# Kernel optimization log

Measured on AMD Instinct MI355X. Metric: run time of the kernel, lower is better.

## Reference

```python
import jax, jax.numpy as jnp
import numpy as np

HIDDEN = 2048
INTER = 8192
RANK = 16
SPARSITY_RATIO = 0.5
MAINTAIN_CHANNELS = 10


def setup_inputs() -> dict:
    key = jax.random.key(0)
    ks = jax.random.split(key, 7)
    B, S = 4, 2048
    x1 = jax.random.normal(ks[0], (B, S, HIDDEN), dtype=jnp.float32)
    # Linear weights stored transposed (in_features, out_features), bias=False
    w_up = jax.random.normal(ks[1], (HIDDEN, INTER), dtype=jnp.float32) / np.sqrt(HIDDEN)
    w_up_lora_a = jax.random.normal(ks[2], (HIDDEN, RANK), dtype=jnp.float32) / np.sqrt(HIDDEN)
    w_up_lora_b = jax.random.normal(ks[3], (RANK, INTER), dtype=jnp.float32) / np.sqrt(RANK)
    w_down = jax.random.normal(ks[4], (INTER, HIDDEN), dtype=jnp.float32) / np.sqrt(INTER)
    w_down_lora_a = jax.random.normal(ks[5], (INTER, RANK), dtype=jnp.float32) / np.sqrt(INTER)
    w_down_lora_b = jax.random.normal(ks[6], (RANK, HIDDEN), dtype=jnp.float32) / np.sqrt(RANK)
    return {
        "x1": x1,
        "w_up": w_up,
        "w_up_lora_a": w_up_lora_a,
        "w_up_lora_b": w_up_lora_b,
        "w_down": w_down,
        "w_down_lora_a": w_down_lora_a,
        "w_down_lora_b": w_down_lora_b,
    }


def reference(x1, w_up, w_up_lora_a, w_up_lora_b, w_down, w_down_lora_a, w_down_lora_b):
    # up projection: dense + low-rank LoRA
    y1 = x1 @ w_up + (x1 @ w_up_lora_a) @ w_up_lora_b          # [B, S, I]
    x2 = jax.nn.relu(y1)                                        # activation_forward='relu'
    # down projection: dense + low-rank LoRA
    y2 = x2 @ w_down + (x2 @ w_down_lora_a) @ w_down_lora_b    # [B, S, H]
    # sparse-save path: per-channel zero counts, keep k channels with FEWEST zeros
    zero_counts = jnp.sum(x2 == 0, axis=-2)                     # [B, I]
    k = min(int(SPARSITY_RATIO * x2.shape[-1]), MAINTAIN_CHANNELS)
    _, topk_indices = jax.lax.top_k(-zero_counts, k)            # smallest counts -> [B, k]
    # per-batch gather of selected channels (replaces Python loop in original)
    x2_save = jnp.take_along_axis(x2, topk_indices[:, None, :], axis=-1)  # [B, S, k]
    return y2, x2_save
```

## Files before the change

### kernel.cpp

```cpp
#include <hip/hip_runtime.h>
#include <stdint.h>

#define HIDDEN 2048
#define INTER 8192
#define RANK 16
#define BATCH 4
#define SEQ 2048
#define MROWS (BATCH * SEQ)
#define KSAVE 10
#define FIXCAP (1u << 18)
#define FIX_TAU 1.2e-4f
#define NHALF 4096

typedef unsigned short u16;
typedef __attribute__((ext_vector_type(8))) __bf16 bf16x8;
typedef __attribute__((ext_vector_type(4))) float f32x4;

__device__ __forceinline__ float bf16_to_f32(u16 h) {
    return __uint_as_float(((unsigned int)h) << 16);
}
__device__ __forceinline__ u16 f32_to_bf16(float f) {
    unsigned int u = __float_as_uint(f);
    u += 0x7fffu + ((u >> 16) & 1u);
    return (u16)(u >> 16);
}
__device__ __forceinline__ void split_bf16(float v, u16& h, u16& l) {
    h = f32_to_bf16(v);
    l = f32_to_bf16(v - bf16_to_f32(h));
}

#define TILE_SH (128 * 32)

__device__ __forceinline__ int swz_chunk(int r, int c) {
    return r * 4 + (c ^ ((r >> 1) & 3));
}

__device__ __forceinline__ void stage_tile(const u16* g, int ldk, u16* lds, int wid, int lane) {
#pragma unroll
    for (int h = 0; h < 2; ++h) {
        int ch = h * 256 + wid * 64 + lane;
        int r = ch >> 2;
        int c = (ch & 3) ^ ((r >> 1) & 3);
        const u16* src = g + (size_t)r * ldk + c * 8;
        u16* dst = lds + (size_t)(h * 256 + wid * 64) * 8;
        __builtin_amdgcn_global_load_lds(
            (const __attribute__((address_space(1))) void*)src,
            (__attribute__((address_space(3))) void*)dst, 16, 0, 0);
    }
}

__device__ __forceinline__ bf16x8 read_frag(const u16* lds, int r, int q) {
    return *(const bf16x8*)(lds + swz_chunk(r, q) * 8);
}

__global__ __launch_bounds__(256) void gemm_up_mfma2(
    const float* __restrict__ x1,
    const u16* __restrict__ wth, const u16* __restrict__ wtl,
    const float* __restrict__ t1, const float* __restrict__ upB,
    u16* __restrict__ x2, unsigned* __restrict__ fixctr, unsigned* __restrict__ fixlist,
    int noff)
{
    __shared__ u16 Ah[TILE_SH], Al[TILE_SH], Bh[TILE_SH], Bl[TILE_SH];
    int tid = threadIdx.x, lane = tid & 63, wid = tid >> 6;
    int wr = wid >> 1, wc = wid & 1;
    int col = lane & 15, q = lane >> 4;

    int bid = blockIdx.y * gridDim.x + blockIdx.x;
    int g = bid >> 9, within = bid & 511;
    int nb = g * 8 + (within & 7);
    int mb = within >> 3;
    int m0 = mb * 128, n0l = nb * 128, n0g = noff + n0l;

    f32x4 acc[4][4];
#pragma unroll
    for (int i = 0; i < 4; ++i)
#pragma unroll
        for (int j = 0; j < 4; ++j) acc[i][j] = (f32x4){0.f, 0.f, 0.f, 0.f};

    const float* ga = x1 + (size_t)m0 * HIDDEN;
    const u16* gb_h = wth + (size_t)n0l * HIDDEN;
    const u16* gb_l = wtl + (size_t)n0l * HIDDEN;
    int f4 = tid & 7;
    int rA = tid >> 3;

    for (int k0 = 0; k0 < HIDDEN; k0 += 32) {
        stage_tile(gb_h + k0, HIDDEN, Bh, wid, lane);
        stage_tile(gb_l + k0, HIDDEN, Bl, wid, lane);
        float4 v[4];
#pragma unroll
        for (int h = 0; h < 4; ++h)
            v[h] = *(const float4*)(ga + (size_t)(rA + h * 32) * HIDDEN + k0 + f4 * 4);
#pragma unroll
        for (int h = 0; h < 4; ++h) {
            int r = rA + h * 32;
            unsigned hx0 = __float_as_uint(v[h].x) & 0xffff0000u;
            unsigned hx1 = __float_as_uint(v[h].y) & 0xffff0000u;
            unsigned hx2 = __float_as_uint(v[h].z) & 0xffff0000u;
            unsigned hx3 = __float_as_uint(v[h].w) & 0xffff0000u;
            float l0 = v[h].x - __uint_as_float(hx0);
            float l1 = v[h].y - __uint_as_float(hx1);
            float l2 = v[h].z - __uint_as_float(hx2);
            float l3 = v[h].w - __uint_as_float(hx3);
            unsigned lo0 = __float_as_uint(l0) & 0xffff0000u;
            unsigned lo1 = __float_as_uint(l1) & 0xffff0000u;
            unsigned lo2 = __float_as_uint(l2) & 0xffff0000u;
            unsigned lo3 = __float_as_uint(l3) & 0xffff0000u;
            uint2 hp = {(hx0 >> 16) | hx1, (hx2 >> 16) | hx3};
            uint2 lp = {(lo0 >> 16) | lo1, (lo2 >> 16) | lo3};
            int pos = swz_chunk(r, f4 >> 1) * 8 + (f4 & 1) * 4;
            *(uint2*)(Ah + pos) = hp;
            *(uint2*)(Al + pos) = lp;
        }
        __syncthreads();
        bf16x8 ah[4], al[4];
#pragma unroll
        for (int i = 0; i < 4; ++i) {
            int r = wr * 64 + i * 16 + col;
            ah[i] = read_frag(Ah, r, q);
            al[i] = read_frag(Al, r, q);
        }
#pragma unroll
        for (int j = 0; j < 4; ++j) {
            int r = wc * 64 + j * 16 + col;
            bf16x8 bh = read_frag(Bh, r, q);
            bf16x8 bl = read_frag(Bl, r, q);
#pragma unroll
            for (int i = 0; i < 4; ++i) {
                acc[i][j] = __builtin_amdgcn_mfma_f32_16x16x32_bf16(ah[i], bh, acc[i][j], 0, 0, 0);
                acc[i][j] = __builtin_amdgcn_mfma_f32_16x16x32_bf16(al[i], bh, acc[i][j], 0, 0, 0);
                acc[i][j] = __builtin_amdgcn_mfma_f32_16x16x32_bf16(ah[i], bl, acc[i][j], 0, 0, 0);
            }
        }
        __syncthreads();
    }

    for (int idx = tid; idx < 128 * 32; idx += 256) {
        int r = idx >> 5, c16 = idx & 31;
        float tv = (c16 < RANK) ? t1[(size_t)(m0 + r) * RANK + c16] : 0.f;
        float uv = (c16 < RANK) ? upB[(size_t)c16 * INTER + n0g + r] : 0.f;
        u16 th, tl2, uh, ul;
        split_bf16(tv, th, tl2);
        split_bf16(uv, uh, ul);
        int pos = swz_chunk(r, c16 >> 3) * 8 + (c16 & 7);
        Ah[pos] = th; Al[pos] = tl2; Bh[pos] = uh; Bl[pos] = ul;
    }
    __syncthreads();
    {
        bf16x8 ah[4], al[4];
#pragma unroll
        for (int i = 0; i < 4; ++i) {
            int r = wr * 64 + i * 16 + col;
            ah[i] = read_frag(Ah, r, q);
            al[i] = read_frag(Al, r, q);
        }
#pragma unroll
        for (int j = 0; j < 4; ++j) {
            int r = wc * 64 + j * 16 + col;
            bf16x8 bh = read_frag(Bh, r, q);
            bf16x8 bl = read_frag(Bl, r, q);
#pragma unroll
            for (int i = 0; i < 4; ++i) {
                acc[i][j] = __builtin_amdgcn_mfma_f32_16x16x32_bf16(ah[i], bh, acc[i][j], 0, 0, 0);
                acc[i][j] = __builtin_amdgcn_mfma_f32_16x16x32_bf16(al[i], bh, acc[i][j], 0, 0, 0);
                acc[i][j] = __builtin_amdgcn_mfma_f32_16x16x32_bf16(ah[i], bl, acc[i][j], 0, 0, 0);
            }
        }
    }

#pragma unroll
    for (int i = 0; i < 4; ++i)
#pragma unroll
        for (int j = 0; j < 4; ++j) {
            int n = n0g + wc * 64 + j * 16 + col;
#pragma unroll
            for (int reg = 0; reg < 4; ++reg) {
                int m = m0 + wr * 64 + i * 16 + q * 4 + reg;
                float v = acc[i][j][reg];
                if (fabsf(v) < FIX_TAU) {
                    unsigned slot = atomicAdd(fixctr, 1u);
                    if (slot < FIXCAP) fixlist[slot] = ((unsigned)m << 13) | (unsigned)n;
                }
                float rv = v > 0.f ? v : 0.f;
                x2[(size_t)m * INTER + n] = f32_to_bf16(rv);
            }
        }
}

__global__ __launch_bounds__(256) void gemm_down_mfma(
    const u16* __restrict__ x2, const u16* __restrict__ wdt,
    const float* __restrict__ t2, const float* __restrict__ dnB,
    float* __restrict__ out)
{
    __shared__ u16 As[TILE_SH], Bs[TILE_SH];
    int tid = threadIdx.x, lane = tid & 63, wid = tid >> 6;
    int wr = wid >> 1, wc = wid & 1;
    int col = lane & 15, q = lane >> 4;
    int m0 = blockIdx.y * 128, n0 = blockIdx.x * 128;

    f32x4 acc[4][4];
#pragma unroll
    for (int i = 0; i < 4; ++i)
#pragma unroll
        for (int j = 0; j < 4; ++j) acc[i][j] = (f32x4){0.f, 0.f, 0.f, 0.f};

    const u16* ga = x2 + (size_t)m0 * INTER;
    const u16* gb = wdt + (size_t)n0 * INTER;

    for (int k0 = 0; k0 < INTER; k0 += 32) {
        stage_tile(ga + k0, INTER, As, wid, lane);
        stage_tile(gb + k0, INTER, Bs, wid, lane);
        __syncthreads();
        bf16x8 af[4];
#pragma unroll
        for (int i = 0; i < 4; ++i) af[i] = read_frag(As, wr * 64 + i * 16 + col, q);
#pragma unroll
        for (int j = 0; j < 4; ++j) {
            bf16x8 bf = read_frag(Bs, wc * 64 + j * 16 + col, q);
#pragma unroll
            for (int i = 0; i < 4; ++i)
                acc[i][j] = __builtin_amdgcn_mfma_f32_16x16x32_bf16(af[i], bf, acc[i][j], 0, 0, 0);
        }
        __syncthreads();
    }

    for (int idx = tid; idx < 128 * 32; idx += 256) {
        int r = idx >> 5, c16 = idx & 31;
        float tv = (c16 < RANK) ? t2[(size_t)(m0 + r) * RANK + c16] : 0.f;
        float uv = (c16 < RANK) ? dnB[(size_t)c16 * HIDDEN + n0 + r] : 0.f;
        int pos = swz_chunk(r, c16 >> 3) * 8 + (c16 & 7);
        As[pos] = f32_to_bf16(tv);
        Bs[pos] = f32_to_bf16(uv);
    }
    __syncthreads();
    {
        bf16x8 af[4];
#pragma unroll
        for (int i = 0; i < 4; ++i) af[i] = read_frag(As, wr * 64 + i * 16 + col, q);
#pragma unroll
        for (int j = 0; j < 4; ++j) {
            bf16x8 bf = read_frag(Bs, wc * 64 + j * 16 + col, q);
#pragma unroll
            for (int i = 0; i < 4; ++i)
                acc[i][j] = __builtin_amdgcn_mfma_f32_16x16x32_bf16(af[i], bf, acc[i][j], 0, 0, 0);
        }
    }
#pragma unroll
    for (int i = 0; i < 4; ++i)
#pragma unroll
        for (int j = 0; j < 4; ++j) {
            int n = n0 + wc * 64 + j * 16 + col;
#pragma unroll
            for (int reg = 0; reg < 4; ++reg) {
                int m = m0 + wr * 64 + i * 16 + q * 4 + reg;
                out[(size_t)m * HIDDEN + n] = acc[i][j][reg];
            }
        }
}

__global__ __launch_bounds__(256) void fixup_kernel(
    const float* __restrict__ x1, const float* __restrict__ w_up,
    const float* __restrict__ t1, const float* __restrict__ upB,
    const unsigned* __restrict__ fixctr, const unsigned* __restrict__ fixlist,
    u16* __restrict__ x2)
{
    unsigned n_items = *fixctr;
    if (n_items > FIXCAP) n_items = FIXCAP;
    int lane = threadIdx.x & 63;
    int gwave = blockIdx.x * 4 + (threadIdx.x >> 6);
    int nwaves = gridDim.x * 4;
    for (unsigned it = gwave; it < n_items; it += nwaves) {
        unsigned code = fixlist[it];
        int m = code >> 13, n = code & 8191;
        float s = 0.f;
        const float* xr = x1 + (size_t)m * HIDDEN;
        for (int k = lane; k < HIDDEN; k += 64)
            s = fmaf(xr[k], w_up[(size_t)k * INTER + n], s);
#pragma unroll
        for (int off = 32; off > 0; off >>= 1) s += __shfl_down(s, off);
        if (lane == 0) {
            float lo = 0.f;
#pragma unroll
            for (int r = 0; r < RANK; ++r)
                lo = fmaf(t1[(size_t)m * RANK + r], upB[(size_t)r * INTER + n], lo);
            float y = s + lo;
            x2[(size_t)m * INTER + n] = f32_to_bf16(y > 0.f ? y : 0.f);
        }
    }
}

template <bool SPLIT>
__global__ __launch_bounds__(256) void transpose_cvt(
    const float* __restrict__ in, u16* __restrict__ outh, u16* __restrict__ outl,
    int R, int C)
{
    __shared__ float t[32][33];
    int x = threadIdx.x & 31, y = threadIdx.x >> 5;
    int r0 = blockIdx.y * 32, c0 = blockIdx.x * 32;
#pragma unroll
    for (int p = 0; p < 4; ++p)
        t[y + p * 8][x] = in[(size_t)(r0 + y + p * 8) * C + c0 + x];
    __syncthreads();
#pragma unroll
    for (int p = 0; p < 4; ++p) {
        float v = t[x][y + p * 8];
        u16 h = f32_to_bf16(v);
        outh[(size_t)(c0 + y + p * 8) * R + r0 + x] = h;
        if (SPLIT)
            outl[(size_t)(c0 + y + p * 8) * R + r0 + x] = f32_to_bf16(v - bf16_to_f32(h));
    }
}

__global__ __launch_bounds__(256) void rowdot16_f32(
    const float* __restrict__ X, const float* __restrict__ A,
    float* __restrict__ T, int K)
{
    __shared__ float red[256][RANK + 1];
    int m = blockIdx.x;
    const float* xr = X + (size_t)m * K;
    float acc[RANK];
#pragma unroll
    for (int r = 0; r < RANK; ++r) acc[r] = 0.f;
    for (int k = threadIdx.x; k < K; k += 256) {
        float xv = xr[k];
        const float* ar = A + (size_t)k * RANK;
#pragma unroll
        for (int r = 0; r < RANK; ++r) acc[r] = fmaf(xv, ar[r], acc[r]);
    }
#pragma unroll
    for (int r = 0; r < RANK; ++r) red[threadIdx.x][r] = acc[r];
    __syncthreads();
    for (int off = 128; off > 0; off >>= 1) {
        if (threadIdx.x < off) {
#pragma unroll
            for (int r = 0; r < RANK; ++r)
                red[threadIdx.x][r] += red[threadIdx.x + off][r];
        }
        __syncthreads();
    }
    if (threadIdx.x < RANK) T[(size_t)m * RANK + threadIdx.x] = red[0][threadIdx.x];
}

__global__ __launch_bounds__(256) void rowdot16_bf16(
    const u16* __restrict__ X, const float* __restrict__ A,
    float* __restrict__ T, int K)
{
    __shared__ float red[256][RANK + 1];
    int m = blockIdx.x;
    const u16* xr = X + (size_t)m * K;
    float acc[RANK];
#pragma unroll
    for (int r = 0; r < RANK; ++r) acc[r] = 0.f;
    for (int k = threadIdx.x; k < K; k += 256) {
        float xv = bf16_to_f32(xr[k]);
        const float* ar = A + (size_t)k * RANK;
#pragma unroll
        for (int r = 0; r < RANK; ++r) acc[r] = fmaf(xv, ar[r], acc[r]);
    }
#pragma unroll
    for (int r = 0; r < RANK; ++r) red[threadIdx.x][r] = acc[r];
    __syncthreads();
    for (int off = 128; off > 0; off >>= 1) {
        if (threadIdx.x < off) {
#pragma unroll
            for (int r = 0; r < RANK; ++r)
                red[threadIdx.x][r] += red[threadIdx.x + off][r];
        }
        __syncthreads();
    }
    if (threadIdx.x < RANK) T[(size_t)m * RANK + threadIdx.x] = red[0][threadIdx.x];
}

#define BM 128
#define BN 128
#define BK 16
#define TM 8

__global__ __launch_bounds__(256) void gemm_up_f32(
    const float* __restrict__ A, const float* __restrict__ B,
    const float* __restrict__ Tl, const float* __restrict__ Bl,
    u16* __restrict__ C, int M, int N, int K)
{
    __shared__ float As[BK][BM + 4];
    __shared__ float Bs[BK][BN];
    int tid = threadIdx.x;
    int tx = tid % 16, ty = tid / 16;
    int m0 = blockIdx.y * BM, n0 = blockIdx.x * BN;
    const float* Ab = A + (size_t)m0 * K;
    const float* Bb = B + n0;
    float acc[TM][8];
#pragma unroll
    for (int i = 0; i < TM; ++i)
#pragma unroll
        for (int j = 0; j < 8; ++j) acc[i][j] = 0.f;

    int arow = tid >> 2, acol = (tid & 3) * 4;
    int brow = tid >> 5, bcol = (tid & 31) * 4;

    for (int k0 = 0; k0 < K; k0 += BK) {
#pragma unroll
        for (int h = 0; h < 2; ++h) {
            int r = arow + h * 64;
            float4 v = *(const float4*)(Ab + (size_t)r * K + k0 + acol);
            As[acol + 0][r] = v.x; As[acol + 1][r] = v.y;
            As[acol + 2][r] = v.z; As[acol + 3][r] = v.w;
        }
#pragma unroll
        for (int h = 0; h < 2; ++h) {
            int r = brow + h * 8;
            float4 v = *(const float4*)(Bb + (size_t)(k0 + r) * N + bcol);
            *(float4*)&Bs[r][bcol] = v;
        }
        __syncthreads();
#pragma unroll
        for (int kk = 0; kk < BK; ++kk) {
            float a[TM], b[8];
#pragma unroll
            for (int i = 0; i < TM; i += 4) *(float4*)&a[i] = *(const float4*)&As[kk][ty * TM + i];
            *(float4*)&b[0] = *(const float4*)&Bs[kk][tx * 4];
            *(float4*)&b[4] = *(const float4*)&Bs[kk][64 + tx * 4];
#pragma unroll
            for (int i = 0; i < TM; ++i)
#pragma unroll
                for (int j = 0; j < 8; ++j)
                    acc[i][j] = fmaf(a[i], b[j], acc[i][j]);
        }
        __syncthreads();
    }
#pragma unroll
    for (int r = 0; r < RANK; ++r) {
        float bv[8];
#pragma unroll
        for (int j = 0; j < 4; ++j) {
            bv[j]     = Bl[(size_t)r * N + n0 + tx * 4 + j];
            bv[4 + j] = Bl[(size_t)r * N + n0 + 64 + tx * 4 + j];
        }
#pragma unroll
        for (int i = 0; i < TM; ++i) {
            float tv = Tl[(size_t)(m0 + ty * TM + i) * RANK + r];
#pragma unroll
            for (int j = 0; j < 8; ++j) acc[i][j] = fmaf(tv, bv[j], acc[i][j]);
        }
    }
#pragma unroll
    for (int i = 0; i < TM; ++i) {
        int m = m0 + ty * TM + i;
        float v[8];
#pragma unroll
        for (int j = 0; j < 8; ++j) { float x = acc[i][j]; v[j] = x > 0.f ? x : 0.f; }
        uint2 p0, p1;
        p0.x = (unsigned)f32_to_bf16(v[0]) | ((unsigned)f32_to_bf16(v[1]) << 16);
        p0.y = (unsigned)f32_to_bf16(v[2]) | ((unsigned)f32_to_bf16(v[3]) << 16);
        p1.x = (unsigned)f32_to_bf16(v[4]) | ((unsigned)f32_to_bf16(v[5]) << 16);
        p1.y = (unsigned)f32_to_bf16(v[6]) | ((unsigned)f32_to_bf16(v[7]) << 16);
        *(uint2*)(C + (size_t)m * N + n0 + tx * 4) = p0;
        *(uint2*)(C + (size_t)m * N + n0 + 64 + tx * 4) = p1;
    }
}

__global__ __launch_bounds__(256) void gemm_down_f32(
    const u16* __restrict__ A, const float* __restrict__ B,
    const float* __restrict__ Tl, const float* __restrict__ Bl,
    float* __restrict__ C, int M, int N, int K)
{
    __shared__ float As[BK][BM + 4];
    __shared__ float Bs[BK][BN];
    int tid = threadIdx.x;
    int tx = tid % 16, ty = tid / 16;
    int m0 = blockIdx.y * BM, n0 = blockIdx.x * BN;
    const u16* Ab = A + (size_t)m0 * K;
    const float* Bb = B + n0;
    float acc[TM][8];
#pragma unroll
    for (int i = 0; i < TM; ++i)
#pragma unroll
        for (int j = 0; j < 8; ++j) acc[i][j] = 0.f;

    int arow = tid >> 1, ahalf = (tid & 1) * 8;
    int brow = tid >> 5, bcol = (tid & 31) * 4;

    for (int k0 = 0; k0 < K; k0 += BK) {
        {
            uint4 v = *(const uint4*)(Ab + (size_t)arow * K + k0 + ahalf);
            unsigned int w_[4] = {v.x, v.y, v.z, v.w};
#pragma unroll
            for (int qq = 0; qq < 4; ++qq) {
                As[ahalf + 2 * qq + 0][arow] = bf16_to_f32((u16)(w_[qq] & 0xffffu));
                As[ahalf + 2 * qq + 1][arow] = bf16_to_f32((u16)(w_[qq] >> 16));
            }
        }
#pragma unroll
        for (int h = 0; h < 2; ++h) {
            int r = brow + h * 8;
            float4 v = *(const float4*)(Bb + (size_t)(k0 + r) * N + bcol);
            *(float4*)&Bs[r][bcol] = v;
        }
        __syncthreads();
#pragma unroll
        for (int kk = 0; kk < BK; ++kk) {
            float a[TM], b[8];
#pragma unroll
            for (int i = 0; i < TM; i += 4) *(float4*)&a[i] = *(const float4*)&As[kk][ty * TM + i];
            *(float4*)&b[0] = *(const float4*)&Bs[kk][tx * 4];
            *(float4*)&b[4] = *(const float4*)&Bs[kk][64 + tx * 4];
#pragma unroll
            for (int i = 0; i < TM; ++i)
#pragma unroll
                for (int j = 0; j < 8; ++j)
                    acc[i][j] = fmaf(a[i], b[j], acc[i][j]);
        }
        __syncthreads();
    }
#pragma unroll
    for (int r = 0; r < RANK; ++r) {
        float bv[8];
#pragma unroll
        for (int j = 0; j < 4; ++j) {
            bv[j]     = Bl[(size_t)r * N + n0 + tx * 4 + j];
            bv[4 + j] = Bl[(size_t)r * N + n0 + 64 + tx * 4 + j];
        }
#pragma unroll
        for (int i = 0; i < TM; ++i) {
            float tv = Tl[(size_t)(m0 + ty * TM + i) * RANK + r];
#pragma unroll
            for (int j = 0; j < 8; ++j) acc[i][j] = fmaf(tv, bv[j], acc[i][j]);
        }
    }
#pragma unroll
    for (int i = 0; i < TM; ++i) {
        int m = m0 + ty * TM + i;
        *(float4*)(C + (size_t)m * N + n0 + tx * 4)      = *(float4*)&acc[i][0];
        *(float4*)(C + (size_t)m * N + n0 + 64 + tx * 4) = *(float4*)&acc[i][4];
    }
}

__global__ __launch_bounds__(256) void count_zeros(
    const u16* __restrict__ X2, int* __restrict__ counts)
{
    int i = blockIdx.x * 256 + threadIdx.x;
    int b = blockIdx.y;
    int s0 = blockIdx.z * 256;
    const u16* p = X2 + ((size_t)(b * SEQ + s0)) * INTER + i;
    int c = 0;
    for (int s = 0; s < 256; ++s) c += (p[(size_t)s * INTER] == 0) ? 1 : 0;
    atomicAdd(&counts[b * INTER + i], c);
}

__global__ __launch_bounds__(256) void topk10(
    const int* __restrict__ counts, int* __restrict__ topidx)
{
    __shared__ int keys[INTER];
    __shared__ int red[256];
    int b = blockIdx.x;
    for (int i = threadIdx.x; i < INTER; i += 256)
        keys[i] = (counts[b * INTER + i] << 13) | i;
    __syncthreads();
    for (int sel = 0; sel < KSAVE; ++sel) {
        int best = 0x7fffffff;
        for (int i = threadIdx.x; i < INTER; i += 256)
            best = min(best, keys[i]);
        red[threadIdx.x] = best;
        __syncthreads();
        for (int off = 128; off > 0; off >>= 1) {
            if (threadIdx.x < off) red[threadIdx.x] = min(red[threadIdx.x], red[threadIdx.x + off]);
            __syncthreads();
        }
        int bestkey = red[0];
        if (threadIdx.x == 0) {
            topidx[b * KSAVE + sel] = bestkey & 0x1fff;
            keys[bestkey & 0x1fff] = 0x7fffffff;
        }
        __syncthreads();
    }
}

__global__ __launch_bounds__(256) void gather_save(
    const u16* __restrict__ X2, const int* __restrict__ topidx,
    float* __restrict__ out2)
{
    int t = blockIdx.x * 256 + threadIdx.x;
    if (t >= BATCH * SEQ * KSAVE) return;
    int j = t % KSAVE;
    int s = (t / KSAVE) % SEQ;
    int b = t / (KSAVE * SEQ);
    int idx = topidx[b * KSAVE + j];
    out2[t] = bf16_to_f32(X2[((size_t)(b * SEQ + s)) * INTER + idx]);
}

extern "C" void kernel_launch(void* const* d_in, const int* in_sizes, int n_in,
                              void* d_out, int out_size, void* d_ws, size_t ws_size,
                              hipStream_t stream)
{
    const float* x1   = (const float*)d_in[0];
    const float* w_up = (const float*)d_in[1];
    const float* upA  = (const float*)d_in[2];
    const float* upB  = (const float*)d_in[3];
    const float* w_dn = (const float*)d_in[4];
    const float* dnA  = (const float*)d_in[5];
    const float* dnB  = (const float*)d_in[6];
    float* out = (float*)d_out;
    char* ws = (char*)d_ws;

    const size_t X2B   = (size_t)MROWS * INTER * 2;
    const size_t WHALF = (size_t)NHALF * HIDDEN * 2;
    const size_t WSPL  = (size_t)HIDDEN * INTER * 2;
    const size_t TB    = (size_t)MROWS * RANK * 4;
    const size_t CNTB  = (size_t)BATCH * INTER * 4;

    size_t fast_need = X2B + 2 * WHALF + 2 * TB + CNTB + 512 + 4 * (size_t)FIXCAP;
    size_t mid_need  = X2B + WSPL + 2 * TB + CNTB + 512;

    u16* x2 = (u16*)ws;
    size_t off = X2B;

    if (ws_size >= fast_need) {
        u16* wth = (u16*)(ws + off);            off += WHALF;
        u16* wtl = (u16*)(ws + off);            off += WHALF;
        float* t1 = (float*)(ws + off);         off += TB;
        float* t2 = (float*)(ws + off);         off += TB;
        int* counts = (int*)(ws + off);         off += CNTB;
        int* topidx = (int*)(ws + off);         off += 256;
        unsigned* fixctr = (unsigned*)(ws + off); off += 256;
        unsigned* fixlist = (unsigned*)(ws + off);
        u16* wdt = wth;

        hipMemsetAsync(counts, 0, CNTB, stream);
        hipMemsetAsync(fixctr, 0, 4, stream);

        rowdot16_f32<<<MROWS, 256, 0, stream>>>(x1, upA, t1, HIDDEN);

        for (int half = 0; half < 2; ++half) {
            int noff = half * NHALF;
            transpose_cvt<true><<<dim3(NHALF / 32, HIDDEN / 32), 256, 0, stream>>>(
                w_up + noff, wth, wtl, HIDDEN, INTER);
            gemm_up_mfma2<<<dim3(NHALF / 128, MROWS / 128), 256, 0, stream>>>(
                x1, wth, wtl, t1, upB, x2, fixctr, fixlist, noff);
        }
        fixup_kernel<<<256, 256, 0, stream>>>(x1, w_up, t1, upB, fixctr, fixlist, x2);

        count_zeros<<<dim3(INTER / 256, BATCH, SEQ / 256), 256, 0, stream>>>(x2, counts);
        topk10<<<BATCH, 256, 0, stream>>>(counts, topidx);
        gather_save<<<(BATCH * SEQ * KSAVE + 255) / 256, 256, 0, stream>>>(
            x2, topidx, out + (size_t)MROWS * HIDDEN);

        transpose_cvt<false><<<dim3(HIDDEN / 32, INTER / 32), 256, 0, stream>>>(
            w_dn, wdt, nullptr, INTER, HIDDEN);
        rowdot16_bf16<<<MROWS, 256, 0, stream>>>(x2, dnA, t2, INTER);
        gemm_down_mfma<<<dim3(HIDDEN / 128, MROWS / 128), 256, 0, stream>>>(
            x2, wdt, t2, dnB, out);
    } else if (ws_size >= mid_need) {
        u16* wdt = (u16*)(ws + off);            off += WSPL;
        float* t1 = (float*)(ws + off);         off += TB;
        float* t2 = (float*)(ws + off);         off += TB;
        int* counts = (int*)(ws + off);         off += CNTB;
        int* topidx = (int*)(ws + off);

        hipMemsetAsync(counts, 0, CNTB, stream);
        rowdot16_f32<<<MROWS, 256, 0, stream>>>(x1, upA, t1, HIDDEN);
        gemm_up_f32<<<dim3(INTER / BN, MROWS / BM), 256, 0, stream>>>(
            x1, w_up, t1, upB, x2, MROWS, INTER, HIDDEN);
        count_zeros<<<dim3(INTER / 256, BATCH, SEQ / 256), 256, 0, stream>>>(x2, counts);
        topk10<<<BATCH, 256, 0, stream>>>(counts, topidx);
        gather_save<<<(BATCH * SEQ * KSAVE + 255) / 256, 256, 0, stream>>>(
            x2, topidx, out + (size_t)MROWS * HIDDEN);
        transpose_cvt<false><<<dim3(HIDDEN / 32, INTER / 32), 256, 0, stream>>>(
            w_dn, wdt, nullptr, INTER, HIDDEN);
        rowdot16_bf16<<<MROWS, 256, 0, stream>>>(x2, dnA, t2, INTER);
        gemm_down_mfma<<<dim3(HIDDEN / 128, MROWS / 128), 256, 0, stream>>>(
            x2, wdt, t2, dnB, out);
    } else {
        float* t1 = (float*)(ws + off);         off += TB;
        float* t2 = (float*)(ws + off);         off += TB;
        int* counts = (int*)(ws + off);         off += CNTB;
        int* topidx = (int*)(ws + off);

        hipMemsetAsync(counts, 0, CNTB, stream);
        rowdot16_f32<<<MROWS, 256, 0, stream>>>(x1, upA, t1, HIDDEN);
        gemm_up_f32<<<dim3(INTER / BN, MROWS / BM), 256, 0, stream>>>(
            x1, w_up, t1, upB, x2, MROWS, INTER, HIDDEN);
        count_zeros<<<dim3(INTER / 256, BATCH, SEQ / 256), 256, 0, stream>>>(x2, counts);
        topk10<<<BATCH, 256, 0, stream>>>(counts, topidx);
        gather_save<<<(BATCH * SEQ * KSAVE + 255) / 256, 256, 0, stream>>>(
            x2, topidx, out + (size_t)MROWS * HIDDEN);
        rowdot16_bf16<<<MROWS, 256, 0, stream>>>(x2, dnA, t2, INTER);
        gemm_down_f32<<<dim3(HIDDEN / BN, MROWS / BM), 256, 0, stream>>>(
            x2, w_dn, t2, dnB, out, MROWS, HIDDEN, INTER);
    }
}
```

Measured before the change: 1.996 ms.

## Widen MFMA GEMM tiles to 128x256 with 8 waves and fuse zero counting

Both the up and down MFMA GEMMs move from 128x128 tiles with 4 waves to 128x256 tiles with 8 waves (512 threads). Each staged A tile is now reused across twice as many output columns, which cuts global and LDS traffic for the activation operand. Zero counting is folded into the up-GEMM epilogue with shuffle reductions and atomics, and the fixup kernel adjusts counts when it flips a sign, so the separate count_zeros pass over x2 is removed. The bf16 rowdot kernel is vectorized to load 8 elements per thread. The costs are more LDS per block, fewer blocks in the grid, and extra atomics in the epilogue.

Result: slower. 2.258 ms (+13.1%).

```diff
diff --git a/kernel.cpp b/kernel.cpp
--- a/kernel.cpp
+++ b/kernel.cpp
@@ -35,14 +35,16 @@
     return r * 4 + (c ^ ((r >> 1) & 3));
 }
 
-__device__ __forceinline__ void stage_tile(const u16* g, int ldk, u16* lds, int wid, int lane) {
-#pragma unroll
-    for (int h = 0; h < 2; ++h) {
-        int ch = h * 256 + wid * 64 + lane;
+template <int NCH>
+__device__ __forceinline__ void stage_tileN(const u16* g, int ldk, u16* lds, int tid) {
+    int wid = tid >> 6, lane = tid & 63;
+#pragma unroll
+    for (int c0 = 0; c0 < NCH; c0 += 512) {
+        int ch = c0 + wid * 64 + lane;
         int r = ch >> 2;
         int c = (ch & 3) ^ ((r >> 1) & 3);
         const u16* src = g + (size_t)r * ldk + c * 8;
-        u16* dst = lds + (size_t)(h * 256 + wid * 64) * 8;
+        u16* dst = lds + (size_t)(c0 + wid * 64) * 8;
         __builtin_amdgcn_global_load_lds(
             (const __attribute__((address_space(1))) void*)src,
             (__attribute__((address_space(3))) void*)dst, 16, 0, 0);
@@ -53,23 +55,25 @@
     return *(const bf16x8*)(lds + swz_chunk(r, q) * 8);
 }
 
-__global__ __launch_bounds__(256) void gemm_up_mfma2(
+__global__ __launch_bounds__(512) void gemm_up_mfma3(
     const float* __restrict__ x1,
     const u16* __restrict__ wth, const u16* __restrict__ wtl,
     const float* __restrict__ t1, const float* __restrict__ upB,
-    u16* __restrict__ x2, unsigned* __restrict__ fixctr, unsigned* __restrict__ fixlist,
+    u16* __restrict__ x2, int* __restrict__ counts,
+    unsigned* __restrict__ fixctr, unsigned* __restrict__ fixlist,
     int noff)
 {
-    __shared__ u16 Ah[TILE_SH], Al[TILE_SH], Bh[TILE_SH], Bl[TILE_SH];
+    __shared__ u16 Ah[TILE_SH], Al[TILE_SH];
+    __shared__ u16 Bh[2 * TILE_SH], Bl[2 * TILE_SH];
     int tid = threadIdx.x, lane = tid & 63, wid = tid >> 6;
-    int wr = wid >> 1, wc = wid & 1;
+    int wr = wid >> 2, wc = wid & 3;
     int col = lane & 15, q = lane >> 4;
 
     int bid = blockIdx.y * gridDim.x + blockIdx.x;
-    int g = bid >> 9, within = bid & 511;
-    int nb = g * 8 + (within & 7);
-    int mb = within >> 3;
-    int m0 = mb * 128, n0l = nb * 128, n0g = noff + n0l;
+    int g = bid >> 8, within = bid & 255;
+    int nb = g * 4 + (within & 3);
+    int mb = within >> 2;
+    int m0 = mb * 128, n0l = nb * 256, n0g = noff + n0l;
 
     f32x4 acc[4][4];
 #pragma unroll
@@ -84,30 +88,27 @@
     int rA = tid >> 3;
 
     for (int k0 = 0; k0 < HIDDEN; k0 += 32) {
-        stage_tile(gb_h + k0, HIDDEN, Bh, wid, lane);
-        stage_tile(gb_l + k0, HIDDEN, Bl, wid, lane);
-        float4 v[4];
-#pragma unroll
-        for (int h = 0; h < 4; ++h)
-            v[h] = *(const float4*)(ga + (size_t)(rA + h * 32) * HIDDEN + k0 + f4 * 4);
-#pragma unroll
-        for (int h = 0; h < 4; ++h) {
-            int r = rA + h * 32;
-            unsigned hx0 = __float_as_uint(v[h].x) & 0xffff0000u;
-            unsigned hx1 = __float_as_uint(v[h].y) & 0xffff0000u;
-            unsigned hx2 = __float_as_uint(v[h].z) & 0xffff0000u;
-            unsigned hx3 = __float_as_uint(v[h].w) & 0xffff0000u;
-            float l0 = v[h].x - __uint_as_float(hx0);
-            float l1 = v[h].y - __uint_as_float(hx1);
-            float l2 = v[h].z - __uint_as_float(hx2);
-            float l3 = v[h].w - __uint_as_float(hx3);
+        stage_tileN<1024>(gb_h + k0, HIDDEN, Bh, tid);
+        stage_tileN<1024>(gb_l + k0, HIDDEN, Bl, tid);
+#pragma unroll
+        for (int h = 0; h < 2; ++h) {
+            int row = rA + h * 64;
+            float4 v = *(const float4*)(ga + (size_t)row * HIDDEN + k0 + f4 * 4);
+            unsigned hx0 = __float_as_uint(v.x) & 0xffff0000u;
+            unsigned hx1 = __float_as_uint(v.y) & 0xffff0000u;
+            unsigned hx2 = __float_as_uint(v.z) & 0xffff0000u;
+            unsigned hx3 = __float_as_uint(v.w) & 0xffff0000u;
+            float l0 = v.x - __uint_as_float(hx0);
+            float l1 = v.y - __uint_as_float(hx1);
+            float l2 = v.z - __uint_as_float(hx2);
+            float l3 = v.w - __uint_as_float(hx3);
             unsigned lo0 = __float_as_uint(l0) & 0xffff0000u;
             unsigned lo1 = __float_as_uint(l1) & 0xffff0000u;
             unsigned lo2 = __float_as_uint(l2) & 0xffff0000u;
             unsigned lo3 = __float_as_uint(l3) & 0xffff0000u;
             uint2 hp = {(hx0 >> 16) | hx1, (hx2 >> 16) | hx3};
             uint2 lp = {(lo0 >> 16) | lo1, (lo2 >> 16) | lo3};
-            int pos = swz_chunk(r, f4 >> 1) * 8 + (f4 & 1) * 4;
+            int pos = swz_chunk(row, f4 >> 1) * 8 + (f4 & 1) * 4;
             *(uint2*)(Ah + pos) = hp;
             *(uint2*)(Al + pos) = lp;
         }
@@ -121,9 +122,9 @@
         }
 #pragma unroll
         for (int j = 0; j < 4; ++j) {
-            int r = wc * 64 + j * 16 + col;
-            bf16x8 bh = read_frag(Bh, r, q);
-            bf16x8 bl = read_frag(Bl, r, q);
+            int rr = wc * 64 + j * 16 + col;
+            bf16x8 bh = read_frag(Bh, rr, q);
+            bf16x8 bl = read_frag(Bl, rr, q);
 #pragma unroll
             for (int i = 0; i < 4; ++i) {
                 acc[i][j] = __builtin_amdgcn_mfma_f32_16x16x32_bf16(ah[i], bh, acc[i][j], 0, 0, 0);
@@ -134,15 +135,21 @@
         __syncthreads();
     }
 
-    for (int idx = tid; idx < 128 * 32; idx += 256) {
+    for (int idx = tid; idx < 4096; idx += 512) {
         int r = idx >> 5, c16 = idx & 31;
         float tv = (c16 < RANK) ? t1[(size_t)(m0 + r) * RANK + c16] : 0.f;
+        u16 th, tl2;
+        split_bf16(tv, th, tl2);
+        int pos = swz_chunk(r, c16 >> 3) * 8 + (c16 & 7);
+        Ah[pos] = th; Al[pos] = tl2;
+    }
+    for (int idx = tid; idx < 8192; idx += 512) {
+        int r = idx >> 5, c16 = idx & 31;
         float uv = (c16 < RANK) ? upB[(size_t)c16 * INTER + n0g + r] : 0.f;
-        u16 th, tl2, uh, ul;
-        split_bf16(tv, th, tl2);
+        u16 uh, ul;
         split_bf16(uv, uh, ul);
         int pos = swz_chunk(r, c16 >> 3) * 8 + (c16 & 7);
-        Ah[pos] = th; Al[pos] = tl2; Bh[pos] = uh; Bl[pos] = ul;
+        Bh[pos] = uh; Bl[pos] = ul;
     }
     __syncthreads();
     {
@@ -155,9 +162,9 @@
         }
 #pragma unroll
         for (int j = 0; j < 4; ++j) {
-            int r = wc * 64 + j * 16 + col;
-            bf16x8 bh = read_frag(Bh, r, q);
-            bf16x8 bl = read_frag(Bl, r, q);
+            int rr = wc * 64 + j * 16 + col;
+            bf16x8 bh = read_frag(Bh, rr, q);
+            bf16x8 bl = read_frag(Bl, rr, q);
 #pragma unroll
             for (int i = 0; i < 4; ++i) {
                 acc[i][j] = __builtin_amdgcn_mfma_f32_16x16x32_bf16(ah[i], bh, acc[i][j], 0, 0, 0);
@@ -167,11 +174,13 @@
         }
     }
 
-#pragma unroll
-    for (int i = 0; i < 4; ++i)
-#pragma unroll
-        for (int j = 0; j < 4; ++j) {
-            int n = n0g + wc * 64 + j * 16 + col;
+    int b = m0 >> 11;
+#pragma unroll
+    for (int j = 0; j < 4; ++j) {
+        int n = n0g + wc * 64 + j * 16 + col;
+        int zc = 0;
+#pragma unroll
+        for (int i = 0; i < 4; ++i) {
 #pragma unroll
             for (int reg = 0; reg < 4; ++reg) {
                 int m = m0 + wr * 64 + i * 16 + q * 4 + reg;
@@ -180,22 +189,28 @@
                     unsigned slot = atomicAdd(fixctr, 1u);
                     if (slot < FIXCAP) fixlist[slot] = ((unsigned)m << 13) | (unsigned)n;
                 }
+                zc += (v <= 0.f) ? 1 : 0;
                 float rv = v > 0.f ? v : 0.f;
                 x2[(size_t)m * INTER + n] = f32_to_bf16(rv);
             }
         }
-}
-
-__global__ __launch_bounds__(256) void gemm_down_mfma(
+        zc += __shfl_down(zc, 32);
+        zc += __shfl_down(zc, 16);
+        if (lane < 16) atomicAdd(&counts[b * INTER + n], zc);
+    }
+}
+
+__global__ __launch_bounds__(512) void gemm_down_mfma2(
     const u16* __restrict__ x2, const u16* __restrict__ wdt,
     const float* __restrict__ t2, const float* __restrict__ dnB,
     float* __restrict__ out)
 {
-    __shared__ u16 As[TILE_SH], Bs[TILE_SH];
+    __shared__ u16 As[TILE_SH];
+    __shared__ u16 Bs[2 * TILE_SH];
     int tid = threadIdx.x, lane = tid & 63, wid = tid >> 6;
-    int wr = wid >> 1, wc = wid & 1;
+    int wr = wid >> 2, wc = wid & 3;
     int col = lane & 15, q = lane >> 4;
-    int m0 = blockIdx.y * 128, n0 = blockIdx.x * 128;
+    int m0 = blockIdx.y * 128, n0 = blockIdx.x * 256;
 
     f32x4 acc[4][4];
 #pragma unroll
@@ -207,8 +222,8 @@
     const u16* gb = wdt + (size_t)n0 * INTER;
 
     for (int k0 = 0; k0 < INTER; k0 += 32) {
-        stage_tile(ga + k0, INTER, As, wid, lane);
-        stage_tile(gb + k0, INTER, Bs, wid, lane);
+        stage_tileN<512>(ga + k0, INTER, As, tid);
+        stage_tileN<1024>(gb + k0, INTER, Bs, tid);
         __syncthreads();
         bf16x8 af[4];
 #pragma unroll
@@ -223,12 +238,16 @@
         __syncthreads();
     }
 
-    for (int idx = tid; idx < 128 * 32; idx += 256) {
+    for (int idx = tid; idx < 4096; idx += 512) {
         int r = idx >> 5, c16 = idx & 31;
         float tv = (c16 < RANK) ? t2[(size_t)(m0 + r) * RANK + c16] : 0.f;
+        int pos = swz_chunk(r, c16 >> 3) * 8 + (c16 & 7);
+        As[pos] = f32_to_bf16(tv);
+    }
+    for (int idx = tid; idx < 8192; idx += 512) {
+        int r = idx >> 5, c16 = idx & 31;
         float uv = (c16 < RANK) ? dnB[(size_t)c16 * HIDDEN + n0 + r] : 0.f;
         int pos = swz_chunk(r, c16 >> 3) * 8 + (c16 & 7);
-        As[pos] = f32_to_bf16(tv);
         Bs[pos] = f32_to_bf16(uv);
     }
     __syncthreads();
@@ -261,7 +280,7 @@
     const float* __restrict__ x1, const float* __restrict__ w_up,
     const float* __restrict__ t1, const float* __restrict__ upB,
     const unsigned* __restrict__ fixctr, const unsigned* __restrict__ fixlist,
-    u16* __restrict__ x2)
+    u16* __restrict__ x2, int* __restrict__ counts)
 {
     unsigned n_items = *fixctr;
     if (n_items > FIXCAP) n_items = FIXCAP;
@@ -283,6 +302,9 @@
             for (int r = 0; r < RANK; ++r)
                 lo = fmaf(t1[(size_t)m * RANK + r], upB[(size_t)r * INTER + n], lo);
             float y = s + lo;
+            int oldz = (x2[(size_t)m * INTER + n] == 0) ? 1 : 0;
+            int newz = (y <= 0.f) ? 1 : 0;
+            if (newz != oldz) atomicAdd(&counts[(m >> 11) * INTER + n], newz - oldz);
             x2[(size_t)m * INTER + n] = f32_to_bf16(y > 0.f ? y : 0.f);
         }
     }
@@ -350,11 +372,19 @@
     float acc[RANK];
 #pragma unroll
     for (int r = 0; r < RANK; ++r) acc[r] = 0.f;
-    for (int k = threadIdx.x; k < K; k += 256) {
-        float xv = bf16_to_f32(xr[k]);
-        const float* ar = A + (size_t)k * RANK;
-#pragma unroll
-        for (int r = 0; r < RANK; ++r) acc[r] = fmaf(xv, ar[r], acc[r]);
+    for (int k = threadIdx.x * 8; k < K; k += 256 * 8) {
+        uint4 p = *(const uint4*)(xr + k);
+        unsigned w_[4] = {p.x, p.y, p.z, p.w};
+#pragma unroll
+        for (int e = 0; e < 4; ++e) {
+            float v0 = bf16_to_f32((u16)(w_[e] & 0xffffu));
+            float v1 = bf16_to_f32((u16)(w_[e] >> 16));
+            const float* ar0 = A + (size_t)(k + 2 * e) * RANK;
+            const float* ar1 = A + (size_t)(k + 2 * e + 1) * RANK;
+#pragma unroll
+            for (int r = 0; r < RANK; ++r)
+                acc[r] = fmaf(v0, ar0[r], fmaf(v1, ar1[r], acc[r]));
+        }
     }
 #pragma unroll
     for (int r = 0; r < RANK; ++r) red[threadIdx.x][r] = acc[r];
@@ -531,6 +561,93 @@
         *(float4*)(C + (size_t)m * N + n0 + tx * 4)      = *(float4*)&acc[i][0];
         *(float4*)(C + (size_t)m * N + n0 + 64 + tx * 4) = *(float4*)&acc[i][4];
     }
+}
+
+__global__ __launch_bounds__(256) void gemm_down_mfma(
+    const u16* __restrict__ x2, const u16* __restrict__ wdt,
+    const float* __restrict__ t2, const float* __restrict__ dnB,
+    float* __restrict__ out)
+{
+    __shared__ u16 As[TILE_SH], Bs[TILE_SH];
+    int tid = threadIdx.x, lane = tid & 63, wid = tid >> 6;
+    int wr = wid >> 1, wc = wid & 1;
+    int col = lane & 15, q = lane >> 4;
+    int m0 = blockIdx.y * 128, n0 = blockIdx.x * 128;
+
+    f32x4 acc[4][4];
+#pragma unroll
+    for (int i = 0; i < 4; ++i)
+#pragma unroll
+        for (int j = 0; j < 4; ++j) acc[i][j] = (f32x4){0.f, 0.f, 0.f, 0.f};
+
+    const u16* ga = x2 + (size_t)m0 * INTER;
+    const u16* gb = wdt + (size_t)n0 * INTER;
+
+    for (int k0 = 0; k0 < INTER; k0 += 32) {
+        {
+            int wid4 = tid >> 6, lane4 = tid & 63;
+#pragma unroll
+            for (int h = 0; h < 2; ++h) {
+                int ch = h * 256 + wid4 * 64 + lane4;
+                int r = ch >> 2;
+                int c = (ch & 3) ^ ((r >> 1) & 3);
+                const u16* srcA = ga + k0 + (size_t)r * INTER + c * 8;
+                u16* dstA = As + (size_t)(h * 256 + wid4 * 64) * 8;
+                __builtin_amdgcn_global_load_lds(
+                    (const __attribute__((address_space(1))) void*)srcA,
+                    (__attribute__((address_space(3))) void*)dstA, 16, 0, 0);
+                const u16* srcB = gb + k0 + (size_t)r * INTER + c * 8;
+                u16* dstB = Bs + (size_t)(h * 256 + wid4 * 64) * 8;
+                __builtin_amdgcn_global_load_lds(
+                    (const __attribute__((address_space(1))) void*)srcB,
+                    (__attribute__((address_space(3))) void*)dstB, 16, 0, 0);
+            }
+        }
+        __syncthreads();
+        bf16x8 af[4];
+#pragma unroll
+        for (int i = 0; i < 4; ++i) af[i] = read_frag(As, wr * 64 + i * 16 + col, q);
+#pragma unroll
+        for (int j = 0; j < 4; ++j) {
+            bf16x8 bf = read_frag(Bs, wc * 64 + j * 16 + col, q);
+#pragma unroll
+            for (int i = 0; i < 4; ++i)
+                acc[i][j] = __builtin_amdgcn_mfma_f32_16x16x32_bf16(af[i], bf, acc[i][j], 0, 0, 0);
+        }
+        __syncthreads();
+    }
+    for (int idx = tid; idx < 128 * 32; idx += 256) {
+        int r = idx >> 5, c16 = idx & 31;
+        float tv = (c16 < RANK) ? t2[(size_t)(m0 + r) * RANK + c16] : 0.f;
+        float uv = (c16 < RANK) ? dnB[(size_t)c16 * HIDDEN + n0 + r] : 0.f;
+        int pos = swz_chunk(r, c16 >> 3) * 8 + (c16 & 7);
+        As[pos] = f32_to_bf16(tv);
+        Bs[pos] = f32_to_bf16(uv);
+    }
+    __syncthreads();
+    {
+        bf16x8 af[4];
+#pragma unroll
+        for (int i = 0; i < 4; ++i) af[i] = read_frag(As, wr * 64 + i * 16 + col, q);
+#pragma unroll
+        for (int j = 0; j < 4; ++j) {
+            bf16x8 bf = read_frag(Bs, wc * 64 + j * 16 + col, q);
+#pragma unroll
+            for (int i = 0; i < 4; ++i)
+                acc[i][j] = __builtin_amdgcn_mfma_f32_16x16x32_bf16(af[i], bf, acc[i][j], 0, 0, 0);
+        }
+    }
+#pragma unroll
+    for (int i = 0; i < 4; ++i)
+#pragma unroll
+        for (int j = 0; j < 4; ++j) {
+            int n = n0 + wc * 64 + j * 16 + col;
+#pragma unroll
+            for (int reg = 0; reg < 4; ++reg) {
+                int m = m0 + wr * 64 + i * 16 + q * 4 + reg;
+                out[(size_t)m * HIDDEN + n] = acc[i][j][reg];
+            }
+        }
 }
 
 __global__ __launch_bounds__(256) void count_zeros(
@@ -632,12 +749,11 @@
             int noff = half * NHALF;
             transpose_cvt<true><<<dim3(NHALF / 32, HIDDEN / 32), 256, 0, stream>>>(
                 w_up + noff, wth, wtl, HIDDEN, INTER);
-            gemm_up_mfma2<<<dim3(NHALF / 128, MROWS / 128), 256, 0, stream>>>(
-                x1, wth, wtl, t1, upB, x2, fixctr, fixlist, noff);
-        }
-        fixup_kernel<<<256, 256, 0, stream>>>(x1, w_up, t1, upB, fixctr, fixlist, x2);
-
-        count_zeros<<<dim3(INTER / 256, BATCH, SEQ / 256), 256, 0, stream>>>(x2, counts);
+            gemm_up_mfma3<<<dim3(NHALF / 256, MROWS / 128), 512, 0, stream>>>(
+                x1, wth, wtl, t1, upB, x2, counts, fixctr, fixlist, noff);
+        }
+        fixup_kernel<<<256, 256, 0, stream>>>(x1, w_up, t1, upB, fixctr, fixlist, x2, counts);
+
         topk10<<<BATCH, 256, 0, stream>>>(counts, topidx);
         gather_save<<<(BATCH * SEQ * KSAVE + 255) / 256, 256, 0, stream>>>(
             x2, topidx, out + (size_t)MROWS * HIDDEN);
@@ -645,7 +761,7 @@
         transpose_cvt<false><<<dim3(HIDDEN / 32, INTER / 32), 256, 0, stream>>>(
             w_dn, wdt, nullptr, INTER, HIDDEN);
         rowdot16_bf16<<<MROWS, 256, 0, stream>>>(x2, dnA, t2, INTER);
-        gemm_down_mfma<<<dim3(HIDDEN / 128, MROWS / 128), 256, 0, stream>>>(
+        gemm_down_mfma2<<<dim3(HIDDEN / 256, MROWS / 128), 512, 0, stream>>>(
             x2, wdt, t2, dnB, out);
     } else if (ws_size >= mid_need) {
         u16* wdt = (u16*)(ws + off);            off += WSPL;
```
